# Kernel optimization log

Measured on AMD Instinct MI355X. Metric: run time of the kernel, lower is better.

## Reference

```python
import jax, jax.numpy as jnp
import numpy as np

HEADS = 8
DIM_HEAD = 64
WINDOW = 256
CAUSAL = True


def _sliding_window_mask(seq_len: int, window: int, causal: bool) -> jnp.ndarray:
    i = jnp.arange(seq_len)[:, None]
    j = jnp.arange(seq_len)[None, :]
    # attend iff i - window + 1 <= j <= i + window - 1 (end_pos exclusive)
    mask = (j >= i - window + 1) & (j <= i + window - 1)
    if causal:
        mask = mask & (j <= i)
    return mask  # (S, S) bool


def setup_inputs() -> dict:
    key = jax.random.key(0)
    k1, k2, k3 = jax.random.split(key, 3)
    dim = 512
    inner = HEADS * DIM_HEAD
    x = jax.random.normal(k1, (2, 2048, dim), dtype=jnp.float32)
    W_qkv = jax.random.normal(k2, (dim, 3 * inner), dtype=jnp.float32) * 0.02
    W_out = jax.random.normal(k3, (inner, dim), dtype=jnp.float32) * 0.02
    return {"x": x, "W_qkv": W_qkv, "W_out": W_out}


def reference(x, W_qkv, W_out):
    B, S, D = x.shape
    H, Dh = HEADS, DIM_HEAD
    scale = Dh ** (-0.5)
    qkv = x @ W_qkv  # (B, S, 3*H*Dh)
    q, k, v = jnp.split(qkv, 3, axis=-1)
    q = q.reshape(B, S, H, Dh).transpose(0, 2, 1, 3)  # (B, H, S, Dh)
    k = k.reshape(B, S, H, Dh).transpose(0, 2, 1, 3)
    v = v.reshape(B, S, H, Dh).transpose(0, 2, 1, 3)
    scores = jnp.einsum('bhid,bhjd->bhij', q, k) * scale
    mask = _sliding_window_mask(S, WINDOW, CAUSAL)
    mask_value = -jnp.finfo(scores.dtype).max
    scores = jnp.where(mask[None, None, :, :], scores, mask_value)
    attn = jax.nn.softmax(scores, axis=-1)  # (B, H, S, S)
    out = jnp.einsum('bhij,bhjd->bhid', attn, v)
    out = out.transpose(0, 2, 1, 3).reshape(B, S, H * Dh)
    out = out @ W_out  # (B, S, D)
    return (out, attn)
```

## Files before the change

### kernel.cpp

```cpp
#include <hip/hip_runtime.h>
#include <hip/hip_bf16.h>

typedef __bf16 bf16x8 __attribute__((ext_vector_type(8)));
typedef float f32x4 __attribute__((ext_vector_type(4)));

#define MFMA16(a,b,c) __builtin_amdgcn_mfma_f32_16x16x32_bf16(a, b, c, 0, 0, 0)

__device__ inline void fill_attn_rows(float* __restrict__ attn, int rowStart, int rowEnd,
                                      int tid) {
  const f32x4 z4 = {0.f, 0.f, 0.f, 0.f};
  for (int g = rowStart; g < rowEnd; g++) {
    const int bh = g >> 11, i = g & 2047;
    const int qt = i >> 6;
    const int lo = qt >= 4 ? (qt - 4) << 6 : 0;
    const int hi = (qt + 1) << 6;
    float* rp = attn + ((size_t)bh << 22) + ((size_t)i << 11);
    for (int j = tid << 2; j < lo; j += 1024)
      __builtin_nontemporal_store(z4, reinterpret_cast<f32x4*>(rp + j));
    for (int j = hi + (tid << 2); j < 2048; j += 1024)
      __builtin_nontemporal_store(z4, reinterpret_cast<f32x4*>(rp + j));
  }
}

__device__ inline void fill_block_chunk(float* __restrict__ attn, int fillStart, int fillEnd,
                                        int fid, int nfill, int tid) {
  const int total = fillEnd - fillStart;
  const int per = (total + nfill - 1) / nfill;
  const int myStart = fillStart + fid * per;
  int myEnd = myStart + per;
  if (myEnd > fillEnd) myEnd = fillEnd;
  if (myStart < myEnd) fill_attn_rows(attn, myStart, myEnd, tid);
}

__device__ inline void transpose_body(const float* __restrict__ in, __bf16* __restrict__ out,
                                      int R, int C, int tile, int tid, float (*t)[65]) {
  const int tilesC = C >> 6;
  const int tc = tile % tilesC, tr = tile / tilesC;
  const int r0 = tr << 6, c0 = tc << 6;
  const int ri = tid >> 2, cq = (tid & 3) << 4;
#pragma unroll
  for (int e = 0; e < 16; e += 4) {
    float4 v = *reinterpret_cast<const float4*>(&in[(size_t)(r0 + ri) * C + c0 + cq + e]);
    t[ri][cq + e]     = v.x;
    t[ri][cq + e + 1] = v.y;
    t[ri][cq + e + 2] = v.z;
    t[ri][cq + e + 3] = v.w;
  }
  __syncthreads();
  const int co = tid >> 2, rq = (tid & 3) << 4;
  __attribute__((aligned(16))) __bf16 buf[16];
#pragma unroll
  for (int e = 0; e < 16; e++) buf[e] = (__bf16)t[rq + e][co];
  *reinterpret_cast<bf16x8*>(&out[(size_t)(c0 + co) * R + r0 + rq])     = *reinterpret_cast<bf16x8*>(&buf[0]);
  *reinterpret_cast<bf16x8*>(&out[(size_t)(c0 + co) * R + r0 + rq + 8]) = *reinterpret_cast<bf16x8*>(&buf[8]);
}

__global__ __launch_bounds__(256) void prep(const float* __restrict__ Wqkv,
                                            const float* __restrict__ Wout,
                                            __bf16* __restrict__ Wqt,
                                            __bf16* __restrict__ Wot) {
  __shared__ float t[64][65];
  const int bid = blockIdx.x, tid = threadIdx.x;
  if (bid < 192) transpose_body(Wqkv, Wqt, 512, 1536, bid, tid, t);
  else           transpose_body(Wout, Wot, 512, 512, bid - 192, tid, t);
}

template <typename AT, typename OT>
__global__ __launch_bounds__(256) void gemm_bt(const AT* __restrict__ A,
                                               const __bf16* __restrict__ Bt,
                                               OT* __restrict__ C, int M, int N, int K,
                                               float* __restrict__ fillAttn,
                                               int fillStart, int fillEnd, int gxCompute) {
  __shared__ __bf16 As[128][72];
  __shared__ __bf16 Bs[128][72];
  const int tid = threadIdx.x;

  if ((int)blockIdx.x >= gxCompute) {
    const int nfx = gridDim.x - gxCompute;
    const int fid = (blockIdx.x - gxCompute) + nfx * blockIdx.y;
    fill_block_chunk(fillAttn, fillStart, fillEnd, fid, nfx * gridDim.y, tid);
    return;
  }

  const int wave = tid >> 6, lane = tid & 63;
  const int c = lane & 15, q4 = lane >> 4;
  const int bm = blockIdx.y << 7, bn = blockIdx.x << 7;
  const int wm = (wave >> 1) << 6, wn = (wave & 1) << 6;
  f32x4 acc[4][4];
#pragma unroll
  for (int m = 0; m < 4; m++)
#pragma unroll
    for (int n = 0; n < 4; n++)
#pragma unroll
      for (int e = 0; e < 4; e++) acc[m][n][e] = 0.f;

  const int srow = tid >> 1, scol = (tid & 1) << 5;
  bf16x8 av[4], bv[4];

  auto loadA = [&](int k0) {
    const AT* ag = A + (size_t)(bm + srow) * K + k0 + scol;
    if constexpr (sizeof(AT) == 4) {
#pragma unroll
      for (int r = 0; r < 4; r++) {
        float4 lo = *reinterpret_cast<const float4*>(ag + r * 8);
        float4 hi = *reinterpret_cast<const float4*>(ag + r * 8 + 4);
        bf16x8 v;
        v[0] = (__bf16)lo.x; v[1] = (__bf16)lo.y; v[2] = (__bf16)lo.z; v[3] = (__bf16)lo.w;
        v[4] = (__bf16)hi.x; v[5] = (__bf16)hi.y; v[6] = (__bf16)hi.z; v[7] = (__bf16)hi.w;
        av[r] = v;
      }
    } else {
#pragma unroll
      for (int r = 0; r < 4; r++) av[r] = *reinterpret_cast<const bf16x8*>(ag + r * 8);
    }
  };
  auto loadB = [&](int k0) {
    const __bf16* bg = Bt + (size_t)(bn + srow) * K + k0 + scol;
#pragma unroll
    for (int r = 0; r < 4; r++) bv[r] = *reinterpret_cast<const bf16x8*>(bg + r * 8);
  };

  loadA(0); loadB(0);
  for (int k0 = 0; k0 < K; k0 += 64) {
    __syncthreads();
#pragma unroll
    for (int r = 0; r < 4; r++) *reinterpret_cast<bf16x8*>(&As[srow][scol + r * 8]) = av[r];
#pragma unroll
    for (int r = 0; r < 4; r++) *reinterpret_cast<bf16x8*>(&Bs[srow][scol + r * 8]) = bv[r];
    __syncthreads();
    if (k0 + 64 < K) { loadA(k0 + 64); loadB(k0 + 64); }
#pragma unroll
    for (int ks = 0; ks < 2; ks++) {
      const int kk = ks * 32 + q4 * 8;
      bf16x8 af[4], bfv[4];
#pragma unroll
      for (int m = 0; m < 4; m++) af[m] = *reinterpret_cast<const bf16x8*>(&As[wm + m * 16 + c][kk]);
#pragma unroll
      for (int n = 0; n < 4; n++) bfv[n] = *reinterpret_cast<const bf16x8*>(&Bs[wn + n * 16 + c][kk]);
#pragma unroll
      for (int m = 0; m < 4; m++)
#pragma unroll
        for (int n = 0; n < 4; n++) acc[m][n] = MFMA16(af[m], bfv[n], acc[m][n]);
    }
  }
#pragma unroll
  for (int m = 0; m < 4; m++)
#pragma unroll
    for (int n = 0; n < 4; n++)
#pragma unroll
      for (int r2 = 0; r2 < 4; r2++) {
        const int row = bm + wm + m * 16 + q4 * 4 + r2;
        const int col = bn + wn + n * 16 + c;
        C[(size_t)row * N + col] = (OT)acc[m][n][r2];
      }
}

__global__ __launch_bounds__(256) void attn_fused(const __bf16* __restrict__ QKV,
                                                  float* __restrict__ attn,
                                                  __bf16* __restrict__ AO) {
  __shared__ __align__(16) __bf16 KV[2][64][72];
  __shared__ __align__(16) __bf16 Pw[4][16][72];
  const int tid = threadIdx.x;

  if (blockIdx.x >= 32) {
    const int fid = (blockIdx.x - 32) + (gridDim.x - 32) * blockIdx.y;
    fill_block_chunk(attn, 9000, 25000, fid, (gridDim.x - 32) * gridDim.y, tid);
    return;
  }

  const int qt = blockIdx.x, bh = blockIdx.y;
  const int b = bh >> 3, h = bh & 7;
  const int qi0 = qt << 6;
  const int wave = tid >> 6, lane = tid & 63;
  const int c = lane & 15, q4 = lane >> 4;
  const int base = b * 2048;
  const int r = tid >> 2, qq = (tid & 3) << 4;

  bf16x8 qf0, qf1;
  {
    const __bf16* s = QKV + (size_t)(base + qi0 + wave * 16 + c) * 1536 + h * 64 + q4 * 8;
    qf0 = *reinterpret_cast<const bf16x8*>(s);
    qf1 = *reinterpret_cast<const bf16x8*>(s + 32);
  }

  f32x4 acc[5][4];
#pragma unroll
  for (int t = 0; t < 5; t++)
#pragma unroll
    for (int ct = 0; ct < 4; ct++)
#pragma unroll
      for (int e = 0; e < 4; e++) acc[t][ct][e] = 0.f;

  const int tfirst = qt >= 4 ? 0 : 4 - qt;
  bf16x8 kv0, kv1;
  {
    const __bf16* s = QKV + (size_t)(base + ((qt - 4 + tfirst) << 6) + r) * 1536 + 512 + h * 64 + qq;
    kv0 = *reinterpret_cast<const bf16x8*>(s);
    kv1 = *reinterpret_cast<const bf16x8*>(s + 8);
  }
  int cur = 0;
#pragma unroll
  for (int t = 0; t < 5; t++) {
    if (qt - 4 + t < 0) continue;
    *reinterpret_cast<bf16x8*>(&KV[cur][r][qq]) = kv0;
    *reinterpret_cast<bf16x8*>(&KV[cur][r][qq + 8]) = kv1;
    if (t < 4) {
      const __bf16* s = QKV + (size_t)(base + ((qt - 3 + t) << 6) + r) * 1536 + 512 + h * 64 + qq;
      kv0 = *reinterpret_cast<const bf16x8*>(s);
      kv1 = *reinterpret_cast<const bf16x8*>(s + 8);
    }
    __syncthreads();
#pragma unroll
    for (int ks = 0; ks < 2; ks++) {
      const int kk = ks * 32 + q4 * 8;
      const bf16x8 af = ks ? qf1 : qf0;
#pragma unroll
      for (int ct = 0; ct < 4; ct++) {
        bf16x8 bfr = *reinterpret_cast<const bf16x8*>(&KV[cur][ct * 16 + c][kk]);
        acc[t][ct] = MFMA16(af, bfr, acc[t][ct]);
      }
    }
    cur ^= 1;
  }

  const float scale = 0.125f;
  const int igBase = qi0 + wave * 16 + q4 * 4;
#pragma unroll
  for (int t = 0; t < 5; t++) {
#pragma unroll
    for (int ct = 0; ct < 4; ct++) {
      const int jb = ((qt - 4 + t) << 6) + ct * 16 + c;
#pragma unroll
      for (int r2 = 0; r2 < 4; r2++) {
        const int ig = igBase + r2;
        const bool valid = (jb >= 0) && (jb <= ig) && (jb >= ig - 255);
        acc[t][ct][r2] = valid ? acc[t][ct][r2] * scale : -1e30f;
      }
    }
  }

  float pm[4];
#pragma unroll
  for (int r2 = 0; r2 < 4; r2++) {
    float v = acc[0][0][r2];
#pragma unroll
    for (int t = 0; t < 5; t++)
#pragma unroll
      for (int ct = 0; ct < 4; ct++) v = fmaxf(v, acc[t][ct][r2]);
    pm[r2] = v;
  }
#pragma unroll
  for (int off = 8; off >= 1; off >>= 1)
#pragma unroll
    for (int r2 = 0; r2 < 4; r2++) pm[r2] = fmaxf(pm[r2], __shfl_xor(pm[r2], off, 64));

  float ps[4] = {0.f, 0.f, 0.f, 0.f};
#pragma unroll
  for (int t = 0; t < 5; t++)
#pragma unroll
    for (int ct = 0; ct < 4; ct++)
#pragma unroll
      for (int r2 = 0; r2 < 4; r2++) {
        float p = __expf(acc[t][ct][r2] - pm[r2]);
        acc[t][ct][r2] = p;
        ps[r2] += p;
      }
#pragma unroll
  for (int off = 8; off >= 1; off >>= 1)
#pragma unroll
    for (int r2 = 0; r2 < 4; r2++) ps[r2] += __shfl_xor(ps[r2], off, 64);

#pragma unroll
  for (int r2 = 0; r2 < 4; r2++) ps[r2] = 1.0f / ps[r2];
#pragma unroll
  for (int t = 0; t < 5; t++)
#pragma unroll
    for (int ct = 0; ct < 4; ct++)
#pragma unroll
      for (int r2 = 0; r2 < 4; r2++) acc[t][ct][r2] *= ps[r2];

  __syncthreads();

  f32x4 o[4];
#pragma unroll
  for (int n = 0; n < 4; n++)
#pragma unroll
    for (int e = 0; e < 4; e++) o[n][e] = 0.f;

  const int jv = tid >> 2, dqa = tid & 3;
  bf16x8 vr0, vr1;
  {
    const __bf16* s = QKV + (size_t)(base + ((qt - 4 + tfirst) << 6) + jv) * 1536 + 1024 + h * 64;
    vr0 = *reinterpret_cast<const bf16x8*>(s + dqa * 8);
    vr1 = *reinterpret_cast<const bf16x8*>(s + (dqa + 4) * 8);
  }
  int pcur = 0;
#pragma unroll
  for (int t = 0; t < 5; t++) {
    if (qt - 4 + t < 0) continue;
#pragma unroll
    for (int ct = 0; ct < 4; ct++)
#pragma unroll
      for (int r2 = 0; r2 < 4; r2++)
        Pw[wave][q4 * 4 + r2][ct * 16 + c] = (__bf16)acc[t][ct][r2];
#pragma unroll
    for (int e = 0; e < 8; e++) {
      KV[pcur][dqa * 8 + e][jv] = vr0[e];
      KV[pcur][(dqa + 4) * 8 + e][jv] = vr1[e];
    }
    if (t < 4) {
      const __bf16* s = QKV + (size_t)(base + ((qt - 3 + t) << 6) + jv) * 1536 + 1024 + h * 64;
      vr0 = *reinterpret_cast<const bf16x8*>(s + dqa * 8);
      vr1 = *reinterpret_cast<const bf16x8*>(s + (dqa + 4) * 8);
    }
    __syncthreads();
#pragma unroll
    for (int ks = 0; ks < 2; ks++) {
      const int kk = ks * 32 + q4 * 8;
      bf16x8 af = *reinterpret_cast<const bf16x8*>(&Pw[wave][c][kk]);
#pragma unroll
      for (int n = 0; n < 4; n++) {
        bf16x8 bfr = *reinterpret_cast<const bf16x8*>(&KV[pcur][n * 16 + c][kk]);
        o[n] = MFMA16(af, bfr, o[n]);
      }
    }
    pcur ^= 1;
  }

  float* arow = attn + ((size_t)bh << 22);
#pragma unroll
  for (int r2 = 0; r2 < 4; r2++) {
    const int ig = igBase + r2;
    float* rowp = arow + ((size_t)ig << 11);
#pragma unroll
    for (int t = 0; t < 5; t++) {
      const int jt0 = (qt - 4 + t) << 6;
      if (jt0 < 0) continue;
#pragma unroll
      for (int ct = 0; ct < 4; ct++) {
        const int jb = jt0 + ct * 16 + c;
        rowp[jb] = acc[t][ct][r2];
      }
    }
  }

#pragma unroll
  for (int n = 0; n < 4; n++)
#pragma unroll
    for (int r2 = 0; r2 < 4; r2++)
      Pw[wave][q4 * 4 + r2][n * 16 + c] = (__bf16)o[n][r2];
  {
    const int er = lane >> 2;
    const int ec = (lane & 3) << 4;
    bf16x8 a0 = *reinterpret_cast<const bf16x8*>(&Pw[wave][er][ec]);
    bf16x8 a1 = *reinterpret_cast<const bf16x8*>(&Pw[wave][er][ec + 8]);
    __bf16* adst = AO + (size_t)(base + qi0 + wave * 16 + er) * 512 + h * 64 + ec;
    *reinterpret_cast<bf16x8*>(adst) = a0;
    *reinterpret_cast<bf16x8*>(adst + 8) = a1;
  }
}

extern "C" void kernel_launch(void* const* d_in, const int* in_sizes, int n_in,
                              void* d_out, int out_size, void* d_ws, size_t ws_size,
                              hipStream_t stream) {
  const float* x = (const float*)d_in[0];
  const float* Wqkv = (const float*)d_in[1];
  const float* Wout = (const float*)d_in[2];
  float* out = (float*)d_out;
  float* attn = out + (size_t)2 * 2048 * 512;

  char* ws = (char*)d_ws;
  __bf16* Wqt  = (__bf16*)(ws);
  __bf16* Wot  = (__bf16*)(ws + 1572864);
  __bf16* QKVb = (__bf16*)(ws + 1572864 + 524288);
  __bf16* AOb  = (__bf16*)(ws + 1572864 + 524288 + 12582912);

  prep<<<256, 256, 0, stream>>>(Wqkv, Wout, Wqt, Wot);

  gemm_bt<float, __bf16><<<dim3(24, 32), 256, 0, stream>>>(x, Wqt, QKVb, 4096, 1536, 512,
                                                           attn, 0, 9000, 12);

  attn_fused<<<dim3(48, 16), 256, 0, stream>>>(QKVb, attn, AOb);

  gemm_bt<__bf16, float><<<dim3(12, 32), 256, 0, stream>>>(AOb, Wot, out, 4096, 512, 512,
                                                           attn, 25000, 32768, 4);
}
```

Baseline: 84.61 us.

## Stage GEMM bf16 tiles via async global_load_lds with XOR-swizzled LDS layout

Replaces register-staged global-to-LDS copies of the bf16 B (and bf16 A) tiles with direct global_load_lds DMA into a dense XOR-swizzled 64-wide LDS layout. The aim is to cut VGPR pressure and staging instructions, and to avoid LDS bank conflicts without padding. The loads are now issued after the first barrier and consumed after the second, so the earlier register prefetch overlap for those operands is lost. It also relies on the second __syncthreads to wait for the async LDS writes, which may need an explicit vmcnt wait to be correct.

Result: no change. 84.81 us (+0.2%).

```diff
diff --git a/kernel.cpp b/kernel.cpp
--- a/kernel.cpp
+++ b/kernel.cpp
@@ -5,6 +5,13 @@
 typedef float f32x4 __attribute__((ext_vector_type(4)));
 
 #define MFMA16(a,b,c) __builtin_amdgcn_mfma_f32_16x16x32_bf16(a, b, c, 0, 0, 0)
+
+typedef const __attribute__((address_space(1))) void* gas_t;
+typedef __attribute__((address_space(3))) void* las_t;
+
+__device__ inline void gload16(const __bf16* g, __bf16* lds) {
+  __builtin_amdgcn_global_load_lds((gas_t)g, (las_t)lds, 16, 0, 0);
+}
 
 __device__ inline void fill_attn_rows(float* __restrict__ attn, int rowStart, int rowEnd,
                                       int tid) {
@@ -71,8 +78,10 @@
                                                OT* __restrict__ C, int M, int N, int K,
                                                float* __restrict__ fillAttn,
                                                int fillStart, int fillEnd, int gxCompute) {
-  __shared__ __bf16 As[128][72];
-  __shared__ __bf16 Bs[128][72];
+  constexpr bool AF32 = (sizeof(AT) == 4);
+  constexpr int ASZ = AF32 ? 128 * 72 * 2 : 128 * 64 * 2;
+  __shared__ __align__(16) char asbuf[ASZ];
+  __shared__ __align__(16) __bf16 BsL[128 * 64];
   const int tid = threadIdx.x;
 
   if ((int)blockIdx.x >= gxCompute) {
@@ -94,49 +103,67 @@
 #pragma unroll
       for (int e = 0; e < 4; e++) acc[m][n][e] = 0.f;
 
+  __bf16 (*AsP)[72] = (AF32 ? (__bf16 (*)[72])asbuf : nullptr);
+  __bf16* AsL = (__bf16*)asbuf;
+
+  const int srow8 = lane >> 3;
+  const int sseg  = lane & 7;
+  auto stage_async = [&](const __bf16* src, __bf16* dst, int rowBase, int k0) {
+#pragma unroll
+    for (int i = 0; i < 4; i++) {
+      const int rb = (wave << 5) + (i << 3);
+      const int rr = rb + srow8;
+      const int cs = sseg ^ (rr & 7);
+      gload16(src + (size_t)(rowBase + rr) * K + k0 + cs * 8, dst + rb * 64);
+    }
+  };
+
   const int srow = tid >> 1, scol = (tid & 1) << 5;
-  bf16x8 av[4], bv[4];
-
-  auto loadA = [&](int k0) {
+  bf16x8 av[4];
+  auto loadA_f32 = [&](int k0) {
     const AT* ag = A + (size_t)(bm + srow) * K + k0 + scol;
-    if constexpr (sizeof(AT) == 4) {
-#pragma unroll
-      for (int r = 0; r < 4; r++) {
-        float4 lo = *reinterpret_cast<const float4*>(ag + r * 8);
-        float4 hi = *reinterpret_cast<const float4*>(ag + r * 8 + 4);
-        bf16x8 v;
-        v[0] = (__bf16)lo.x; v[1] = (__bf16)lo.y; v[2] = (__bf16)lo.z; v[3] = (__bf16)lo.w;
-        v[4] = (__bf16)hi.x; v[5] = (__bf16)hi.y; v[6] = (__bf16)hi.z; v[7] = (__bf16)hi.w;
-        av[r] = v;
-      }
-    } else {
-#pragma unroll
-      for (int r = 0; r < 4; r++) av[r] = *reinterpret_cast<const bf16x8*>(ag + r * 8);
+#pragma unroll
+    for (int r = 0; r < 4; r++) {
+      float4 lo = *reinterpret_cast<const float4*>(ag + r * 8);
+      float4 hi = *reinterpret_cast<const float4*>(ag + r * 8 + 4);
+      bf16x8 v;
+      v[0] = (__bf16)lo.x; v[1] = (__bf16)lo.y; v[2] = (__bf16)lo.z; v[3] = (__bf16)lo.w;
+      v[4] = (__bf16)hi.x; v[5] = (__bf16)hi.y; v[6] = (__bf16)hi.z; v[7] = (__bf16)hi.w;
+      av[r] = v;
     }
   };
-  auto loadB = [&](int k0) {
-    const __bf16* bg = Bt + (size_t)(bn + srow) * K + k0 + scol;
-#pragma unroll
-    for (int r = 0; r < 4; r++) bv[r] = *reinterpret_cast<const bf16x8*>(bg + r * 8);
-  };
-
-  loadA(0); loadB(0);
+
+  if constexpr (AF32) loadA_f32(0);
+
   for (int k0 = 0; k0 < K; k0 += 64) {
     __syncthreads();
-#pragma unroll
-    for (int r = 0; r < 4; r++) *reinterpret_cast<bf16x8*>(&As[srow][scol + r * 8]) = av[r];
-#pragma unroll
-    for (int r = 0; r < 4; r++) *reinterpret_cast<bf16x8*>(&Bs[srow][scol + r * 8]) = bv[r];
+    if constexpr (AF32) {
+#pragma unroll
+      for (int r = 0; r < 4; r++)
+        *reinterpret_cast<bf16x8*>(&AsP[srow][scol + r * 8]) = av[r];
+    } else {
+      stage_async((const __bf16*)A, AsL, bm, k0);
+    }
+    stage_async(Bt, BsL, bn, k0);
     __syncthreads();
-    if (k0 + 64 < K) { loadA(k0 + 64); loadB(k0 + 64); }
+    if constexpr (AF32) {
+      if (k0 + 64 < K) loadA_f32(k0 + 64);
+    }
 #pragma unroll
     for (int ks = 0; ks < 2; ks++) {
       const int kk = ks * 32 + q4 * 8;
       bf16x8 af[4], bfv[4];
 #pragma unroll
-      for (int m = 0; m < 4; m++) af[m] = *reinterpret_cast<const bf16x8*>(&As[wm + m * 16 + c][kk]);
-#pragma unroll
-      for (int n = 0; n < 4; n++) bfv[n] = *reinterpret_cast<const bf16x8*>(&Bs[wn + n * 16 + c][kk]);
+      for (int m = 0; m < 4; m++) {
+        const int row = wm + m * 16 + c;
+        if constexpr (AF32) af[m] = *reinterpret_cast<const bf16x8*>(&AsP[row][kk]);
+        else af[m] = *reinterpret_cast<const bf16x8*>(&AsL[row * 64 + ((ks * 4 + q4) ^ (row & 7)) * 8]);
+      }
+#pragma unroll
+      for (int n = 0; n < 4; n++) {
+        const int row = wn + n * 16 + c;
+        bfv[n] = *reinterpret_cast<const bf16x8*>(&BsL[row * 64 + ((ks * 4 + q4) ^ (row & 7)) * 8]);
+      }
 #pragma unroll
       for (int m = 0; m < 4; m++)
 #pragma unroll
```
